# Optimization experiments

Hardware: AMD Instinct MI355X
Metric: run time of the kernel (lower is better)

## Reference

```python
import jax, jax.numpy as jnp
import numpy as np

# TuckerLinear: in_features = out_features = 4096, num_modes = 3
IN_SHAPE = (16, 16, 16)    # get_shape(4096, 3)
OUT_SHAPE = (16, 16, 16)
IN_FEATURES = 4096
OUT_FEATURES = 4096


def setup_inputs() -> dict:
    key = jax.random.key(0)
    ks = jax.random.split(key, 12)
    B, S = 4, 4096
    x = jax.random.normal(ks[0], (B, S, IN_FEATURES), dtype=jnp.float32)
    core = jax.random.normal(ks[1], (8, 8, 8, 8, 8, 8), dtype=jnp.float32) * 0.05
    fi0 = jax.random.normal(ks[2], (16, 8), dtype=jnp.float32) * 0.3
    fi1 = jax.random.normal(ks[3], (16, 8), dtype=jnp.float32) * 0.3
    fi2 = jax.random.normal(ks[4], (16, 8), dtype=jnp.float32) * 0.3
    fo0 = jax.random.normal(ks[5], (16, 8), dtype=jnp.float32) * 0.3
    fo1 = jax.random.normal(ks[6], (16, 8), dtype=jnp.float32) * 0.3
    fo2 = jax.random.normal(ks[7], (16, 8), dtype=jnp.float32) * 0.3
    bias = jax.random.normal(ks[8], (OUT_FEATURES,), dtype=jnp.float32) * 0.01
    per_dim_scale = jnp.ones((OUT_FEATURES,), dtype=jnp.float32)
    alpha = jnp.ones((1,), dtype=jnp.float32)
    input_perm = jax.random.permutation(ks[9], IN_FEATURES).astype(jnp.int32)
    return dict(x=x, core=core, fi0=fi0, fi1=fi1, fi2=fi2,
                fo0=fo0, fo1=fo1, fo2=fo2,
                per_dim_scale=per_dim_scale, alpha=alpha, bias=bias,
                input_perm=input_perm)


def reference(x, core, fi0, fi1, fi2, fo0, fo1, fo2,
              per_dim_scale, alpha, bias, input_perm):
    batch_dims = x.shape[:-1]
    # 1. input channel permutation (spectral reordering)
    xp = jnp.take(x, input_perm, axis=-1)
    # 2. reshape to expose input modes: (N, 16, 16, 16)
    t = xp.reshape(-1, *IN_SHAPE)
    # 3. contract each input mode with its factor (16 -> 8)
    t = jnp.einsum('nabc,ap->npbc', t, fi0)
    t = jnp.einsum('npbc,bq->npqc', t, fi1)
    t = jnp.einsum('npqc,cr->npqr', t, fi2)
    # 4. contract with core over all input-rank modes: (N,8,8,8) -> (N,8,8,8)
    t = jnp.einsum('npqr,xyzpqr->nxyz', t, core)
    # 5. contract each output mode with its factor (8 -> 16)
    t = jnp.einsum('nxyz,Xx->nXyz', t, fo0)
    t = jnp.einsum('nXyz,Yy->nXYz', t, fo1)
    t = jnp.einsum('nXYz,Zz->nXYZ', t, fo2)
    # 6. flatten output modes, scale, bias
    out = t.reshape(-1, OUT_FEATURES)
    out = out * per_dim_scale * alpha + bias
    return out.reshape(*batch_dims, OUT_FEATURES)
```

## Files before the change

### kernel.cpp

```cpp
#include <hip/hip_runtime.h>
#include <stdint.h>

#define NROWS 16384
#define D 4096

typedef __bf16 bf16x8 __attribute__((ext_vector_type(8)));
typedef float  f32x4  __attribute__((ext_vector_type(4)));

__device__ inline unsigned short f2bf(float f) {
    unsigned u = __float_as_uint(f);
    u += 0x7fffu + ((u >> 16) & 1u);
    return (unsigned short)(u >> 16);
}

__global__ __launch_bounds__(256) void k_corebf(const float* __restrict__ core,
                                                unsigned int* __restrict__ cb) {
    const int o = blockIdx.x;
    const int kp = threadIdx.x;
    float2 v = *(const float2*)&core[o * 512 + 2 * kp];
    cb[((size_t)(kp >> 2) * 512 + o) * 4 + (kp & 3)] =
        (unsigned)f2bf(v.x) | ((unsigned)f2bf(v.y) << 16);
}

__global__ __launch_bounds__(256, 5) void k_t3(const float* __restrict__ x,
                                               const float* __restrict__ fi0,
                                               const float* __restrict__ fi1,
                                               const float* __restrict__ fi2,
                                               const int* __restrict__ perm,
                                               unsigned int* __restrict__ t3out) {
    __shared__ float xr[4096];
    __shared__ float t1[2048];
    __shared__ float t2[1024];
    __shared__ float fac[3][128];

    const int tid = threadIdx.x;
    const int n = blockIdx.x;

    {
        const int h = tid & 127;
        fac[0][h] = fi0[h];
        fac[1][h] = fi1[h];
        fac[2][h] = fi2[h];
    }
    int pj[16];
    #pragma unroll
    for (int j = 0; j < 16; ++j) pj[j] = perm[j * 256 + tid];

    {
        const float4* src = (const float4*)(x + (size_t)n * D);
        #pragma unroll
        for (int i = 0; i < 4; ++i) {
            const int c = i * 256 + tid;
            __builtin_amdgcn_global_load_lds(
                (const __attribute__((address_space(1))) void*)(src + c),
                (__attribute__((address_space(3))) void*)(&xr[c * 4]),
                16, 0, 0);
        }
    }
    asm volatile("s_waitcnt vmcnt(0) lgkmcnt(0)" ::: "memory");
    __builtin_amdgcn_s_barrier();

    {
        float a8[8] = {0,0,0,0,0,0,0,0};
        #pragma unroll
        for (int a = 0; a < 16; ++a) {
            float v = xr[pj[a]];
            #pragma unroll
            for (int p = 0; p < 8; ++p) a8[p] += v * fac[0][a * 8 + p];
        }
        #pragma unroll
        for (int p = 0; p < 8; ++p) t1[p * 256 + tid] = a8[p];
    }
    asm volatile("s_waitcnt lgkmcnt(0)" ::: "memory");
    __builtin_amdgcn_s_barrier();

    {
        const int p = tid >> 5, c = (tid >> 1) & 15, qh = tid & 1;
        float a4[4] = {0,0,0,0};
        #pragma unroll
        for (int b = 0; b < 16; ++b) {
            float v = t1[p * 256 + b * 16 + c];
            #pragma unroll
            for (int qi = 0; qi < 4; ++qi) a4[qi] += v * fac[1][b * 8 + qh * 4 + qi];
        }
        #pragma unroll
        for (int qi = 0; qi < 4; ++qi) t2[p * 128 + (qh * 4 + qi) * 16 + c] = a4[qi];
    }
    asm volatile("s_waitcnt lgkmcnt(0)" ::: "memory");
    __builtin_amdgcn_s_barrier();

    {
        const int p = tid >> 5, q = (tid >> 2) & 7, rh = tid & 3;
        float a2[2] = {0,0};
        #pragma unroll
        for (int c = 0; c < 16; ++c) {
            float v = t2[p * 128 + q * 16 + c];
            #pragma unroll
            for (int ri = 0; ri < 2; ++ri) a2[ri] += v * fac[2][c * 8 + rh * 2 + ri];
        }
        const int kt = tid >> 5, k4 = (tid >> 2) & 7, w = tid & 3;
        t3out[(((size_t)kt * 8 + k4) * NROWS + n) * 4 + w] =
            (unsigned)f2bf(a2[0]) | ((unsigned)f2bf(a2[1]) << 16);
    }
}

__global__ __launch_bounds__(256, 2) void k_core(const __bf16* __restrict__ t3,
                                                 const __bf16* __restrict__ cb,
                                                 unsigned short* __restrict__ t4) {
    __shared__ __bf16 lA[2][8192];
    __shared__ __bf16 lB[2][8192];

    const int tid = threadIdx.x, lane = tid & 63, wv = tid >> 6;

    const int bid = blockIdx.x;
    const int wgid = (bid & 7) * 64 + (bid >> 3);
    const int m0 = (wgid >> 2) * 128;
    const int n0 = (wgid & 3) * 128;
    const int wm = wv >> 1, wn = wv & 1;
    const int l15 = lane & 15, l4 = lane >> 4;

    auto stage = [&](int b, int kt) {
        #pragma unroll
        for (int i = 0; i < 4; ++i) {
            const int c = i * 256 + tid;
            const int k4 = c >> 7, r = c & 127;
            const __bf16* ga = t3 + ((size_t)(kt * 8 + k4) * NROWS + m0 + r) * 8;
            __builtin_amdgcn_global_load_lds(
                (const __attribute__((address_space(1))) void*)ga,
                (__attribute__((address_space(3))) void*)(&lA[b][(size_t)c * 8]),
                16, 0, 0);
            const __bf16* gb = cb + ((size_t)(kt * 8 + k4) * 512 + n0 + r) * 8;
            __builtin_amdgcn_global_load_lds(
                (const __attribute__((address_space(1))) void*)gb,
                (__attribute__((address_space(3))) void*)(&lB[b][(size_t)c * 8]),
                16, 0, 0);
        }
    };

    f32x4 acc[4][4] = {};

    auto compute = [&](int cur) {
        #pragma unroll
        for (int kk = 0; kk < 2; ++kk) {
            const int k4f = kk * 4 + l4;
            bf16x8 af[4], bfr[4];
            #pragma unroll
            for (int mt = 0; mt < 4; ++mt)
                af[mt] = *(const bf16x8*)&lA[cur][(k4f * 128 + wm * 64 + mt * 16 + l15) * 8];
            #pragma unroll
            for (int nt = 0; nt < 4; ++nt)
                bfr[nt] = *(const bf16x8*)&lB[cur][(k4f * 128 + wn * 64 + nt * 16 + l15) * 8];
            #pragma unroll
            for (int mt = 0; mt < 4; ++mt)
                #pragma unroll
                for (int nt = 0; nt < 4; ++nt)
                    acc[mt][nt] = __builtin_amdgcn_mfma_f32_16x16x32_bf16(
                        af[mt], bfr[nt], acc[mt][nt], 0, 0, 0);
        }
    };

    stage(0, 0);
    stage(1, 1);
    #pragma unroll 1
    for (int kt = 0; kt < 8; ++kt) {
        if (kt < 7) asm volatile("s_waitcnt vmcnt(8)" ::: "memory");
        else        asm volatile("s_waitcnt vmcnt(0)" ::: "memory");
        __builtin_amdgcn_s_barrier();
        __builtin_amdgcn_s_setprio(1);
        compute(kt & 1);
        __builtin_amdgcn_s_setprio(0);
        __builtin_amdgcn_s_barrier();
        if (kt < 6) stage(kt & 1, kt + 2);
    }

    #pragma unroll
    for (int nt = 0; nt < 4; ++nt) {
        const int col = n0 + wn * 64 + nt * 16 + l15;
        #pragma unroll
        for (int mt = 0; mt < 4; ++mt) {
            const int row = m0 + wm * 64 + mt * 16 + l4 * 4;
            #pragma unroll
            for (int j = 0; j < 4; ++j)
                t4[(size_t)(row + j) * 512 + col] = f2bf(acc[mt][nt][j]);
        }
    }
}

__global__ __launch_bounds__(256, 2) void k_expand(const unsigned short* __restrict__ t4,
                                                   const float* __restrict__ fo0,
                                                   const float* __restrict__ fo1,
                                                   const float* __restrict__ fo2,
                                                   const float* __restrict__ pds,
                                                   const float* __restrict__ alphap,
                                                   const float* __restrict__ bias,
                                                   float* __restrict__ out) {
    __shared__ __bf16 t4L[4][2][512];
    __shared__ float  t5L[4][1024];
    __shared__ float  t6L[4][2304];
    __shared__ float  fo0L[128];

    const int tid = threadIdx.x, w = tid >> 6, l = tid & 63;
    const int n0 = blockIdx.x * 32 + w * 8;
    const int ly = l >> 3, lz = l & 7;
    const int lq = l & 3, lx = l >> 2;

    if (tid < 128) fo0L[tid] = fo0[tid];
    const float alpha = alphap[0];

    float fo1f[2][8];
    #pragma unroll
    for (int h = 0; h < 2; ++h) {
        f32x4 a = *(const f32x4*)&fo1[(h * 8 + ly) * 8];
        f32x4 b = *(const f32x4*)&fo1[(h * 8 + ly) * 8 + 4];
        #pragma unroll
        for (int j = 0; j < 4; ++j) { fo1f[h][j] = a[j]; fo1f[h][4 + j] = b[j]; }
    }
    float fo2s[4][8];
    #pragma unroll
    for (int j = 0; j < 4; ++j) {
        f32x4 a = *(const f32x4*)&fo2[(lq * 4 + j) * 8];
        f32x4 b = *(const f32x4*)&fo2[(lq * 4 + j) * 8 + 4];
        #pragma unroll
        for (int zz = 0; zz < 4; ++zz) { fo2s[j][zz] = a[zz]; fo2s[j][4 + zz] = b[zz]; }
    }

    auto stage = [&](int b, int n) {
        const unsigned short* src = t4 + (size_t)n * 512 + l * 8;
        __builtin_amdgcn_global_load_lds(
            (const __attribute__((address_space(1))) void*)src,
            (__attribute__((address_space(3))) void*)(&t4L[w][b][l * 8]),
            16, 0, 0);
    };

    stage(0, n0);
    asm volatile("s_waitcnt vmcnt(0) lgkmcnt(0)" ::: "memory");
    __syncthreads();

    #pragma unroll 1
    for (int r = 0; r < 8; ++r) {
        const int b = r & 1;
        if (r) asm volatile("s_waitcnt vmcnt(48)" ::: "memory");

        float rv[8];
        #pragma unroll
        for (int xx = 0; xx < 8; ++xx)
            rv[xx] = (float)t4L[w][b][xx * 64 + l];
        if (r + 1 < 8) stage(b ^ 1, n0 + r + 1);
        #pragma unroll
        for (int X = 0; X < 16; ++X) {
            f32x4 f0 = *(const f32x4*)&fo0L[X * 8];
            f32x4 f1 = *(const f32x4*)&fo0L[X * 8 + 4];
            float s = rv[0] * f0[0] + rv[1] * f0[1] + rv[2] * f0[2] + rv[3] * f0[3]
                    + rv[4] * f1[0] + rv[5] * f1[1] + rv[6] * f1[2] + rv[7] * f1[3];
            t5L[w][X * 64 + lz * 8 + ly] = s;
        }
        asm volatile("s_waitcnt lgkmcnt(0)" ::: "memory");

        #pragma unroll
        for (int X = 0; X < 16; ++X) {
            f32x4 u0 = *(const f32x4*)&t5L[w][X * 64 + lz * 8];
            f32x4 u1 = *(const f32x4*)&t5L[w][X * 64 + lz * 8 + 4];
            float a0 = u0[0] * fo1f[0][0] + u0[1] * fo1f[0][1] + u0[2] * fo1f[0][2] + u0[3] * fo1f[0][3]
                     + u1[0] * fo1f[0][4] + u1[1] * fo1f[0][5] + u1[2] * fo1f[0][6] + u1[3] * fo1f[0][7];
            float a1 = u0[0] * fo1f[1][0] + u0[1] * fo1f[1][1] + u0[2] * fo1f[1][2] + u0[3] * fo1f[1][3]
                     + u1[0] * fo1f[1][4] + u1[1] * fo1f[1][5] + u1[2] * fo1f[1][6] + u1[3] * fo1f[1][7];
            t6L[w][(X * 16 + ly) * 9 + lz]     = a0;
            t6L[w][(X * 16 + ly + 8) * 9 + lz] = a1;
        }
        asm volatile("s_waitcnt lgkmcnt(0)" ::: "memory");

        float* orow = out + (size_t)(n0 + r) * 4096;
        #pragma unroll
        for (int c2 = 0; c2 < 16; ++c2) {
            const int XY = c2 * 16 + lx;
            f32x4 pq = *(const f32x4*)&pds[c2 * 256 + l * 4];
            f32x4 bq = *(const f32x4*)&bias[c2 * 256 + l * 4];
            float tv[8];
            #pragma unroll
            for (int zz = 0; zz < 8; ++zz) tv[zz] = t6L[w][XY * 9 + zz];
            f32x4 o4;
            #pragma unroll
            for (int j = 0; j < 4; ++j) {
                float t7 = tv[0] * fo2s[j][0] + tv[1] * fo2s[j][1]
                         + tv[2] * fo2s[j][2] + tv[3] * fo2s[j][3]
                         + tv[4] * fo2s[j][4] + tv[5] * fo2s[j][5]
                         + tv[6] * fo2s[j][6] + tv[7] * fo2s[j][7];
                o4[j] = t7 * (pq[j] * alpha) + bq[j];
            }
            *(f32x4*)&orow[c2 * 256 + l * 4] = o4;
        }
    }
}

extern "C" void kernel_launch(void* const* d_in, const int* in_sizes, int n_in,
                              void* d_out, int out_size, void* d_ws, size_t ws_size,
                              hipStream_t stream) {
    const float* x     = (const float*)d_in[0];
    const float* core  = (const float*)d_in[1];
    const float* fi0   = (const float*)d_in[2];
    const float* fi1   = (const float*)d_in[3];
    const float* fi2   = (const float*)d_in[4];
    const float* fo0   = (const float*)d_in[5];
    const float* fo1   = (const float*)d_in[6];
    const float* fo2   = (const float*)d_in[7];
    const float* pds   = (const float*)d_in[8];
    const float* alpha = (const float*)d_in[9];
    const float* bias  = (const float*)d_in[10];
    const int*   perm  = (const int*)d_in[11];
    float* outp = (float*)d_out;

    char* ws = (char*)d_ws;
    unsigned int*   cb   = (unsigned int*)(ws);
    unsigned int*   t3ws = (unsigned int*)(ws + 1048576);
    unsigned short* t4   = (unsigned short*)(ws + 17825792);

    k_corebf<<<512, 256, 0, stream>>>(core, cb);
    k_t3<<<NROWS, 256, 0, stream>>>(x, fi0, fi1, fi2, perm, t3ws);
    k_core<<<512, 256, 0, stream>>>((const __bf16*)t3ws, (const __bf16*)cb, t4);
    k_expand<<<512, 256, 0, stream>>>(t4, fo0, fo1, fo2, pds, alpha, bias, outp);
}
```

Before: 167.8 us.

## Restructure expand kernel: permuted t4 layout, direct register loads, bf16 LDS, more blocks

The core GEMM epilogue now writes t4 in a permuted column order, so each lane of the expand kernel can load its 8 x-values as one contiguous 16-byte vector straight into registers. This replaces the global_load_lds double-buffering. The intermediate t6 tile is stored in LDS as bf16 instead of fp32, shrinking shared memory. Each wave now handles 4 rows instead of 8, with the grid doubled to 1024 blocks and launch bounds raised to 4 blocks per CU, to get more occupancy and parallelism. The extra bf16 rounding of the intermediate adds numerical error, and the permuted epilogue stores may coalesce less well.

```diff
diff --git a/kernel.cpp b/kernel.cpp
--- a/kernel.cpp
+++ b/kernel.cpp
@@ -176,17 +176,18 @@
     #pragma unroll
     for (int nt = 0; nt < 4; ++nt) {
         const int col = n0 + wn * 64 + nt * 16 + l15;
+        const int oo = (col & 63) * 8 + (col >> 6);
         #pragma unroll
         for (int mt = 0; mt < 4; ++mt) {
             const int row = m0 + wm * 64 + mt * 16 + l4 * 4;
             #pragma unroll
             for (int j = 0; j < 4; ++j)
-                t4[(size_t)(row + j) * 512 + col] = f2bf(acc[mt][nt][j]);
-        }
-    }
-}
-
-__global__ __launch_bounds__(256, 2) void k_expand(const unsigned short* __restrict__ t4,
+                t4[(size_t)(row + j) * 512 + oo] = f2bf(acc[mt][nt][j]);
+        }
+    }
+}
+
+__global__ __launch_bounds__(256, 4) void k_expand(const unsigned short* __restrict__ t4,
                                                    const float* __restrict__ fo0,
                                                    const float* __restrict__ fo1,
                                                    const float* __restrict__ fo2,
@@ -194,13 +195,12 @@
                                                    const float* __restrict__ alphap,
                                                    const float* __restrict__ bias,
                                                    float* __restrict__ out) {
-    __shared__ __bf16 t4L[4][2][512];
-    __shared__ float  t5L[4][1024];
-    __shared__ float  t6L[4][2304];
-    __shared__ float  fo0L[128];
+    __shared__ float          t5L[4][1024];
+    __shared__ unsigned short t6L[4][2560];
+    __shared__ float          fo0L[128];
 
     const int tid = threadIdx.x, w = tid >> 6, l = tid & 63;
-    const int n0 = blockIdx.x * 32 + w * 8;
+    const int n0 = blockIdx.x * 16 + w * 4;
     const int ly = l >> 3, lz = l & 7;
     const int lq = l & 3, lx = l >> 2;
 
@@ -224,28 +224,10 @@
         for (int zz = 0; zz < 4; ++zz) { fo2s[j][zz] = a[zz]; fo2s[j][4 + zz] = b[zz]; }
     }
 
-    auto stage = [&](int b, int n) {
-        const unsigned short* src = t4 + (size_t)n * 512 + l * 8;
-        __builtin_amdgcn_global_load_lds(
-            (const __attribute__((address_space(1))) void*)src,
-            (__attribute__((address_space(3))) void*)(&t4L[w][b][l * 8]),
-            16, 0, 0);
-    };
-
-    stage(0, n0);
-    asm volatile("s_waitcnt vmcnt(0) lgkmcnt(0)" ::: "memory");
-    __syncthreads();
-
-    #pragma unroll 1
-    for (int r = 0; r < 8; ++r) {
-        const int b = r & 1;
-        if (r) asm volatile("s_waitcnt vmcnt(48)" ::: "memory");
-
+    auto ROW = [&](bf16x8 vcur, int r) {
         float rv[8];
         #pragma unroll
-        for (int xx = 0; xx < 8; ++xx)
-            rv[xx] = (float)t4L[w][b][xx * 64 + l];
-        if (r + 1 < 8) stage(b ^ 1, n0 + r + 1);
+        for (int xx = 0; xx < 8; ++xx) rv[xx] = (float)vcur[xx];
         #pragma unroll
         for (int X = 0; X < 16; ++X) {
             f32x4 f0 = *(const f32x4*)&fo0L[X * 8];
@@ -264,8 +246,8 @@
                      + u1[0] * fo1f[0][4] + u1[1] * fo1f[0][5] + u1[2] * fo1f[0][6] + u1[3] * fo1f[0][7];
             float a1 = u0[0] * fo1f[1][0] + u0[1] * fo1f[1][1] + u0[2] * fo1f[1][2] + u0[3] * fo1f[1][3]
                      + u1[0] * fo1f[1][4] + u1[1] * fo1f[1][5] + u1[2] * fo1f[1][6] + u1[3] * fo1f[1][7];
-            t6L[w][(X * 16 + ly) * 9 + lz]     = a0;
-            t6L[w][(X * 16 + ly + 8) * 9 + lz] = a1;
+            t6L[w][(X * 16 + ly) * 10 + lz]      = f2bf(a0);
+            t6L[w][(X * 16 + ly + 8) * 10 + lz]  = f2bf(a1);
         }
         asm volatile("s_waitcnt lgkmcnt(0)" ::: "memory");
 
@@ -277,7 +259,11 @@
             f32x4 bq = *(const f32x4*)&bias[c2 * 256 + l * 4];
             float tv[8];
             #pragma unroll
-            for (int zz = 0; zz < 8; ++zz) tv[zz] = t6L[w][XY * 9 + zz];
+            for (int k = 0; k < 4; ++k) {
+                unsigned u = *(const unsigned*)&t6L[w][XY * 10 + 2 * k];
+                tv[2 * k]     = __uint_as_float(u << 16);
+                tv[2 * k + 1] = __uint_as_float(u & 0xffff0000u);
+            }
             f32x4 o4;
             #pragma unroll
             for (int j = 0; j < 4; ++j) {
@@ -289,7 +275,18 @@
             }
             *(f32x4*)&orow[c2 * 256 + l * 4] = o4;
         }
-    }
+        asm volatile("s_waitcnt lgkmcnt(0)" ::: "memory");
+    };
+
+    bf16x8 v0 = *(const bf16x8*)(t4 + (size_t)(n0 + 0) * 512 + l * 8);
+    bf16x8 v1 = *(const bf16x8*)(t4 + (size_t)(n0 + 1) * 512 + l * 8);
+    __syncthreads();
+    bf16x8 v2 = *(const bf16x8*)(t4 + (size_t)(n0 + 2) * 512 + l * 8);
+    bf16x8 v3 = *(const bf16x8*)(t4 + (size_t)(n0 + 3) * 512 + l * 8);
+    ROW(v0, 0);
+    ROW(v1, 1);
+    ROW(v2, 2);
+    ROW(v3, 3);
 }
 
 extern "C" void kernel_launch(void* const* d_in, const int* in_sizes, int n_in,
@@ -317,5 +314,5 @@
     k_corebf<<<512, 256, 0, stream>>>(core, cb);
     k_t3<<<NROWS, 256, 0, stream>>>(x, fi0, fi1, fi2, perm, t3ws);
     k_core<<<512, 256, 0, stream>>>((const __bf16*)t3ws, (const __bf16*)cb, t4);
-    k_expand<<<512, 256, 0, stream>>>(t4, fo0, fo1, fo2, pds, alpha, bias, outp);
-}
+    k_expand<<<1024, 256, 0, stream>>>(t4, fo0, fo1, fo2, pds, alpha, bias, outp);
+}
```

Measured after the change: 185.6 us. +10.7%, slower.
